# Performance work log

Hardware: AMD Instinct MI355X
Metric: run time of the kernel (lower is better)

Reference implementation:

```python
import jax, jax.numpy as jnp
import numpy as np

N, C, T, V = 128, 256, 64, 32
FILTERS = 256

def setup_inputs() -> dict:
    key = jax.random.key(0)
    k1, k2, k3 = jax.random.split(key, 3)
    x = jax.random.normal(k1, (N, C, T, V), dtype=jnp.float32)
    a = jax.random.uniform(k2, (N, T, V, V), dtype=jnp.float32)
    # 1x1 Conv2D (channels_first) == pointwise channel projection: weight [C_in, filters]
    W = jax.random.normal(k3, (C, FILTERS), dtype=jnp.float32) * (2.0 / FILTERS) ** 0.5
    b = jnp.zeros((FILTERS,), dtype=jnp.float32)
    return {"x": x, "a": a, "W": W, "b": b}

def reference(x, a, W, b):
    # 1x1 conv over channels_first input: [n,c,t,v] -> [n,f,t,v]
    h = jnp.einsum('nctv,cf->nftv', x, W) + b[None, :, None, None]
    # Dropout is identity at inference (training=False).
    # Per-frame graph convolution: contract vertex dim with adjacency.
    out = jnp.einsum('nctv,ntvw->nctw', h, a)
    return (out, a)
```

## Files before the change

kernel.cpp:

```cpp
#include <hip/hip_runtime.h>


#define NN 128
#define CC 256
#define TT 64
#define VV 32
#define FF 256
#define TB 4

typedef _Float16 half8 __attribute__((ext_vector_type(8)));
typedef _Float16 half4 __attribute__((ext_vector_type(4)));
typedef float floatx4 __attribute__((ext_vector_type(4)));

__global__ __launch_bounds__(256) void wt_prep_kernel(const float* __restrict__ W,
                                                      _Float16* __restrict__ Wt) {
    const int c = blockIdx.x;
    const int f = threadIdx.x;
    Wt[f * CC + c] = (_Float16)W[c * FF + f];
}

__global__ __launch_bounds__(512, 2) void sgcn_mfma10_kernel(
    const float* __restrict__ x, const float* __restrict__ a,
    const _Float16* __restrict__ Wt, const float* __restrict__ b,
    float* __restrict__ out, float* __restrict__ out_a)
{
    __shared__ _Float16 a_t[TB * VV * VV];
    __shared__ _Float16 g_s[TB * VV * 256];
    __shared__ float    s_lds[TB][VV];

    const int tid  = threadIdx.x;
    const int lane = tid & 63;
    const int wv   = tid >> 6;
    const int l15  = lane & 15;
    const int lg   = lane >> 4;
    const int blk  = blockIdx.x;
    const int n    = blk >> 4;
    const int t0   = (blk & 15) * TB;

    char* at_base = (char*)a_t;
    char* g_base  = (char*)g_s;

    const int tA    = wv >> 1;
    const int chalf = wv & 1;

    float4 xf[16];
    #pragma unroll
    for (int ci = 0; ci < 8; ++ci) {
        const int c = (chalf * 8 + ci) * 16 + l15;
        const float* xp = x + (((size_t)n * CC + c) * TT + (t0 + tA)) * VV + 8 * lg;
        xf[ci * 2 + 0] = *reinterpret_cast<const float4*>(xp);
        xf[ci * 2 + 1] = *reinterpret_cast<const float4*>(xp + 4);
    }

    #pragma unroll
    for (int k = 0; k < 2; ++k) {
        const int o  = (tid + 512 * k) * 4;
        const int it = o >> 10;
        const int r  = o & 1023;
        const int v  = r >> 5;
        const int w0 = r & 31;
        const size_t off = ((size_t)(n * TT + t0 + it)) * (VV * VV) + r;
        float4 av = *reinterpret_cast<const float4*>(a + off);
        *reinterpret_cast<float4*>(out_a + off) = av;
        #pragma unroll
        for (int j = 0; j < 4; ++j) {
            const int row = it * VV + w0 + j;
            const float e = j == 0 ? av.x : j == 1 ? av.y : j == 2 ? av.z : av.w;
            *reinterpret_cast<_Float16*>(at_base + row * 64 +
                                         ((v * 2) ^ ((row & 3) << 4))) = (_Float16)e;
        }
    }

    __syncthreads();

    if (tid < TB * VV) {
        const int it = tid >> 5, w = tid & 31;
        const int row = it * VV + w;
        float ss = 0.0f;
        #pragma unroll
        for (int v = 0; v < VV; ++v)
            ss += (float)*reinterpret_cast<const _Float16*>(
                at_base + row * 64 + ((v * 2) ^ ((row & 3) << 4)));
        s_lds[it][w] = ss;
    }

    {
        const int r0 = tA * VV + l15, r1 = r0 + 16;
        half8 bA0 = *reinterpret_cast<const half8*>(at_base + r0 * 64 +
                                                    ((16 * lg) ^ ((r0 & 3) << 4)));
        half8 bA1 = *reinterpret_cast<const half8*>(at_base + r1 * 64 +
                                                    ((16 * lg) ^ ((r1 & 3) << 4)));
        char* gt = g_base + tA * (VV * 256 * 2);
        #pragma unroll
        for (int ci = 0; ci < 8; ++ci) {
            const int ct = chalf * 8 + ci;
            half8 af;
            float4 x0 = xf[ci * 2 + 0], x1 = xf[ci * 2 + 1];
            af[0] = (_Float16)x0.x; af[1] = (_Float16)x0.y;
            af[2] = (_Float16)x0.z; af[3] = (_Float16)x0.w;
            af[4] = (_Float16)x1.x; af[5] = (_Float16)x1.y;
            af[6] = (_Float16)x1.z; af[7] = (_Float16)x1.w;
            #pragma unroll
            for (int wt = 0; wt < 2; ++wt) {
                floatx4 acc = {0.f, 0.f, 0.f, 0.f};
                acc = __builtin_amdgcn_mfma_f32_16x16x32_f16(af, wt ? bA1 : bA0, acc, 0, 0, 0);
                half4 gh;
                gh[0] = (_Float16)acc[0]; gh[1] = (_Float16)acc[1];
                gh[2] = (_Float16)acc[2]; gh[3] = (_Float16)acc[3];
                const int row = 16 * wt + l15;
                const int cb  = (ct * 16 + 4 * lg) * 2;
                *reinterpret_cast<half4*>(gt + row * 512 + (cb ^ ((row & 7) << 4))) = gh;
            }
        }
    }
    __syncthreads();

    #pragma unroll
    for (int fth = 0; fth < 2; ++fth) {
        const int ft = fth * 8 + wv;
        const int f  = ft * 16 + l15;
        half8 wb[8];
        const _Float16* wp = Wt + (size_t)f * CC + 8 * lg;
        #pragma unroll
        for (int ks = 0; ks < 8; ++ks)
            wb[ks] = *reinterpret_cast<const half8*>(wp + 32 * ks);
        const float bvf = b[f];

        #pragma unroll
        for (int tt = 0; tt < TB; ++tt) {
            char* gt = g_base + tt * (VV * 256 * 2);
            floatx4 acc2[2];
            acc2[0] = (floatx4){0.f, 0.f, 0.f, 0.f};
            acc2[1] = (floatx4){0.f, 0.f, 0.f, 0.f};

            __builtin_amdgcn_s_setprio(1);
            #pragma unroll
            for (int ks = 0; ks < 8; ++ks) {
                const int r0 = l15, r1 = 16 + l15;
                const int cb = (32 * ks + 8 * lg) * 2;
                half8 ga0 = *reinterpret_cast<const half8*>(gt + r0 * 512 +
                                                            (cb ^ ((r0 & 7) << 4)));
                half8 ga1 = *reinterpret_cast<const half8*>(gt + r1 * 512 +
                                                            (cb ^ ((r1 & 7) << 4)));
                acc2[0] = __builtin_amdgcn_mfma_f32_16x16x32_f16(ga0, wb[ks], acc2[0], 0, 0, 0);
                acc2[1] = __builtin_amdgcn_mfma_f32_16x16x32_f16(ga1, wb[ks], acc2[1], 0, 0, 0);
            }
            __builtin_amdgcn_s_setprio(0);

            float* ob = out + (((size_t)n * FF + f) * TT + (t0 + tt)) * VV;
            #pragma unroll
            for (int mt = 0; mt < 2; ++mt) {
                const int w0 = 16 * mt + 4 * lg;
                float4 sv = *reinterpret_cast<const float4*>(&s_lds[tt][w0]);
                float4 o;
                o.x = acc2[mt][0] + bvf * sv.x;
                o.y = acc2[mt][1] + bvf * sv.y;
                o.z = acc2[mt][2] + bvf * sv.z;
                o.w = acc2[mt][3] + bvf * sv.w;
                *reinterpret_cast<float4*>(ob + w0) = o;
            }
        }
    }
}

__global__ __launch_bounds__(256) void sgcn_fused_kernel(
    const float* __restrict__ x, const float* __restrict__ a,
    const float* __restrict__ W, const float* __restrict__ b,
    float* __restrict__ out, float* __restrict__ out_a)
{
    __shared__ float x_lds[CC][VV];
    __shared__ float a_lds[VV][VV];
    const int tid = threadIdx.x;
    const int nt  = blockIdx.x;
    const int n   = nt >> 6;
    const int t   = nt & 63;
    const float* xb = x + (size_t)n * CC * TT * VV + (size_t)t * VV;
    #pragma unroll
    for (int k = 0; k < 8; ++k) {
        int e = tid * 4 + k * 1024;
        int c = e >> 5, v = e & 31;
        float4 val = *reinterpret_cast<const float4*>(xb + (size_t)c * (TT * VV) + v);
        *reinterpret_cast<float4*>(&x_lds[c][v]) = val;
    }
    {
        const float* ab = a + (size_t)nt * (VV * VV);
        float4 av = *reinterpret_cast<const float4*>(ab + tid * 4);
        *reinterpret_cast<float4*>(&a_lds[0][0] + tid * 4) = av;
        *reinterpret_cast<float4*>(out_a + (size_t)nt * (VV * VV) + tid * 4) = av;
    }
    __syncthreads();
    const int f = tid;
    float h[VV];
    #pragma unroll
    for (int v = 0; v < VV; ++v) h[v] = 0.0f;
    #pragma unroll 4
    for (int c = 0; c < CC; ++c) {
        float wv = W[c * FF + f];
        #pragma unroll
        for (int v = 0; v < VV; ++v) h[v] = fmaf(x_lds[c][v], wv, h[v]);
    }
    const float bias = b[f];
    #pragma unroll
    for (int v = 0; v < VV; ++v) h[v] += bias;
    float o[VV];
    #pragma unroll
    for (int w = 0; w < VV; ++w) o[w] = 0.0f;
    #pragma unroll
    for (int v = 0; v < VV; ++v) {
        float hv = h[v];
        #pragma unroll
        for (int w = 0; w < VV; ++w) o[w] = fmaf(hv, a_lds[v][w], o[w]);
    }
    float* ob = out + (((size_t)n * FF + f) * TT + t) * VV;
    #pragma unroll
    for (int w = 0; w < VV; w += 4)
        *reinterpret_cast<float4*>(ob + w) = make_float4(o[w], o[w+1], o[w+2], o[w+3]);
}

extern "C" void kernel_launch(void* const* d_in, const int* in_sizes, int n_in,
                              void* d_out, int out_size, void* d_ws, size_t ws_size,
                              hipStream_t stream) {
    const float* x = (const float*)d_in[0];
    const float* a = (const float*)d_in[1];
    const float* W = (const float*)d_in[2];
    const float* b = (const float*)d_in[3];

    float* out   = (float*)d_out;
    float* out_a = out + (size_t)NN * FF * TT * VV;

    const size_t wt_bytes = (size_t)FF * CC * sizeof(_Float16);

    if (ws_size >= wt_bytes) {
        _Float16* Wt = (_Float16*)d_ws;
        wt_prep_kernel<<<dim3(CC), dim3(FF), 0, stream>>>(W, Wt);
        sgcn_mfma10_kernel<<<dim3(NN * (TT / TB)), dim3(512), 0, stream>>>(x, a, Wt, b, out, out_a);
    } else {
        sgcn_fused_kernel<<<dim3(NN * TT), dim3(256), 0, stream>>>(x, a, W, b, out, out_a);
    }
}
```

Measured before the change: 145.7 us.

## Make blocks persistent over four time chunks with software-prefetched x and adjacency loads

Each block now loops over four consecutive time-chunks instead of handling one. Half of the next chunk's x tile and its adjacency tile are prefetched into registers while the current chunk's second GEMM runs, so global-load latency overlaps with MFMA work. The grid shrinks fourfold (512 blocks), which lowers launch parallelism and may reduce latency hiding on a large GPU. W fragments are still reloaded for every chunk, and the extra prefetch registers raise register pressure.

```diff
diff --git a/kernel.cpp b/kernel.cpp
--- a/kernel.cpp
+++ b/kernel.cpp
@@ -7,6 +7,7 @@
 #define VV 32
 #define FF 256
 #define TB 4
+#define NCH 4
 
 typedef _Float16 half8 __attribute__((ext_vector_type(8)));
 typedef _Float16 half4 __attribute__((ext_vector_type(4)));
@@ -19,14 +20,14 @@
     Wt[f * CC + c] = (_Float16)W[c * FF + f];
 }
 
-__global__ __launch_bounds__(512, 2) void sgcn_mfma10_kernel(
+__global__ __launch_bounds__(512, 2) void sgcn_mfma12_kernel(
     const float* __restrict__ x, const float* __restrict__ a,
     const _Float16* __restrict__ Wt, const float* __restrict__ b,
     float* __restrict__ out, float* __restrict__ out_a)
 {
     __shared__ _Float16 a_t[TB * VV * VV];
     __shared__ _Float16 g_s[TB * VV * 256];
-    __shared__ float    s_lds[TB][VV];
+    __shared__ float    s_buf[2][TB][VV];
 
     const int tid  = threadIdx.x;
     const int lane = tid & 63;
@@ -34,8 +35,8 @@
     const int l15  = lane & 15;
     const int lg   = lane >> 4;
     const int blk  = blockIdx.x;
-    const int n    = blk >> 4;
-    const int t0   = (blk & 15) * TB;
+    const int n    = blk >> 2;
+    const int tgb  = (blk & 3) * NCH;
 
     char* at_base = (char*)a_t;
     char* g_base  = (char*)g_s;
@@ -43,121 +44,160 @@
     const int tA    = wv >> 1;
     const int chalf = wv & 1;
 
-    float4 xf[16];
-    #pragma unroll
-    for (int ci = 0; ci < 8; ++ci) {
-        const int c = (chalf * 8 + ci) * 16 + l15;
-        const float* xp = x + (((size_t)n * CC + c) * TT + (t0 + tA)) * VV + 8 * lg;
-        xf[ci * 2 + 0] = *reinterpret_cast<const float4*>(xp);
-        xf[ci * 2 + 1] = *reinterpret_cast<const float4*>(xp + 4);
-    }
-
-    #pragma unroll
-    for (int k = 0; k < 2; ++k) {
-        const int o  = (tid + 512 * k) * 4;
-        const int it = o >> 10;
-        const int r  = o & 1023;
-        const int v  = r >> 5;
-        const int w0 = r & 31;
-        const size_t off = ((size_t)(n * TT + t0 + it)) * (VV * VV) + r;
-        float4 av = *reinterpret_cast<const float4*>(a + off);
-        *reinterpret_cast<float4*>(out_a + off) = av;
-        #pragma unroll
-        for (int j = 0; j < 4; ++j) {
-            const int row = it * VV + w0 + j;
-            const float e = j == 0 ? av.x : j == 1 ? av.y : j == 2 ? av.z : av.w;
-            *reinterpret_cast<_Float16*>(at_base + row * 64 +
-                                         ((v * 2) ^ ((row & 3) << 4))) = (_Float16)e;
-        }
-    }
-
-    __syncthreads();
-
-    if (tid < TB * VV) {
-        const int it = tid >> 5, w = tid & 31;
-        const int row = it * VV + w;
-        float ss = 0.0f;
-        #pragma unroll
-        for (int v = 0; v < VV; ++v)
-            ss += (float)*reinterpret_cast<const _Float16*>(
-                at_base + row * 64 + ((v * 2) ^ ((row & 3) << 4)));
-        s_lds[it][w] = ss;
-    }
-
+    const int o0  = tid * 4;
+    const int o1  = (tid + 512) * 4;
+    const int it0 = o0 >> 10, r0s = o0 & 1023;
+    const int it1 = o1 >> 10, r1s = o1 & 1023;
+
+    float4 a_nx[2];
+    float4 xp[8];
     {
-        const int r0 = tA * VV + l15, r1 = r0 + 16;
-        half8 bA0 = *reinterpret_cast<const half8*>(at_base + r0 * 64 +
-                                                    ((16 * lg) ^ ((r0 & 3) << 4)));
-        half8 bA1 = *reinterpret_cast<const half8*>(at_base + r1 * 64 +
-                                                    ((16 * lg) ^ ((r1 & 3) << 4)));
-        char* gt = g_base + tA * (VV * 256 * 2);
-        #pragma unroll
-        for (int ci = 0; ci < 8; ++ci) {
-            const int ct = chalf * 8 + ci;
-            half8 af;
-            float4 x0 = xf[ci * 2 + 0], x1 = xf[ci * 2 + 1];
-            af[0] = (_Float16)x0.x; af[1] = (_Float16)x0.y;
-            af[2] = (_Float16)x0.z; af[3] = (_Float16)x0.w;
-            af[4] = (_Float16)x1.x; af[5] = (_Float16)x1.y;
-            af[6] = (_Float16)x1.z; af[7] = (_Float16)x1.w;
-            #pragma unroll
-            for (int wt = 0; wt < 2; ++wt) {
-                floatx4 acc = {0.f, 0.f, 0.f, 0.f};
-                acc = __builtin_amdgcn_mfma_f32_16x16x32_f16(af, wt ? bA1 : bA0, acc, 0, 0, 0);
-                half4 gh;
-                gh[0] = (_Float16)acc[0]; gh[1] = (_Float16)acc[1];
-                gh[2] = (_Float16)acc[2]; gh[3] = (_Float16)acc[3];
-                const int row = 16 * wt + l15;
-                const int cb  = (ct * 16 + 4 * lg) * 2;
-                *reinterpret_cast<half4*>(gt + row * 512 + (cb ^ ((row & 7) << 4))) = gh;
-            }
-        }
-    }
-    __syncthreads();
-
-    #pragma unroll
-    for (int fth = 0; fth < 2; ++fth) {
-        const int ft = fth * 8 + wv;
-        const int f  = ft * 16 + l15;
-        half8 wb[8];
-        const _Float16* wp = Wt + (size_t)f * CC + 8 * lg;
-        #pragma unroll
-        for (int ks = 0; ks < 8; ++ks)
-            wb[ks] = *reinterpret_cast<const half8*>(wp + 32 * ks);
-        const float bvf = b[f];
-
-        #pragma unroll
-        for (int tt = 0; tt < TB; ++tt) {
-            char* gt = g_base + tt * (VV * 256 * 2);
-            floatx4 acc2[2];
-            acc2[0] = (floatx4){0.f, 0.f, 0.f, 0.f};
-            acc2[1] = (floatx4){0.f, 0.f, 0.f, 0.f};
-
-            __builtin_amdgcn_s_setprio(1);
-            #pragma unroll
-            for (int ks = 0; ks < 8; ++ks) {
-                const int r0 = l15, r1 = 16 + l15;
-                const int cb = (32 * ks + 8 * lg) * 2;
-                half8 ga0 = *reinterpret_cast<const half8*>(gt + r0 * 512 +
-                                                            (cb ^ ((r0 & 7) << 4)));
-                half8 ga1 = *reinterpret_cast<const half8*>(gt + r1 * 512 +
-                                                            (cb ^ ((r1 & 7) << 4)));
-                acc2[0] = __builtin_amdgcn_mfma_f32_16x16x32_f16(ga0, wb[ks], acc2[0], 0, 0, 0);
-                acc2[1] = __builtin_amdgcn_mfma_f32_16x16x32_f16(ga1, wb[ks], acc2[1], 0, 0, 0);
-            }
-            __builtin_amdgcn_s_setprio(0);
-
-            float* ob = out + (((size_t)n * FF + f) * TT + (t0 + tt)) * VV;
-            #pragma unroll
-            for (int mt = 0; mt < 2; ++mt) {
-                const int w0 = 16 * mt + 4 * lg;
-                float4 sv = *reinterpret_cast<const float4*>(&s_lds[tt][w0]);
-                float4 o;
-                o.x = acc2[mt][0] + bvf * sv.x;
-                o.y = acc2[mt][1] + bvf * sv.y;
-                o.z = acc2[mt][2] + bvf * sv.z;
-                o.w = acc2[mt][3] + bvf * sv.w;
-                *reinterpret_cast<float4*>(ob + w0) = o;
+        const int t0 = tgb * TB;
+        a_nx[0] = *reinterpret_cast<const float4*>(a + ((size_t)(n * TT + t0 + it0)) * 1024 + r0s);
+        a_nx[1] = *reinterpret_cast<const float4*>(a + ((size_t)(n * TT + t0 + it1)) * 1024 + r1s);
+        #pragma unroll
+        for (int ci = 0; ci < 4; ++ci) {
+            const int c = (chalf * 8 + ci) * 16 + l15;
+            const float* xpp = x + (((size_t)n * CC + c) * TT + (t0 + tA)) * VV + 8 * lg;
+            xp[ci * 2 + 0] = *reinterpret_cast<const float4*>(xpp);
+            xp[ci * 2 + 1] = *reinterpret_cast<const float4*>(xpp + 4);
+        }
+    }
+
+    #pragma unroll 1
+    for (int ch = 0; ch < NCH; ++ch) {
+        const int t0 = (tgb + ch) * TB;
+
+        float4 xb[8];
+        #pragma unroll
+        for (int ci = 4; ci < 8; ++ci) {
+            const int c = (chalf * 8 + ci) * 16 + l15;
+            const float* xpp = x + (((size_t)n * CC + c) * TT + (t0 + tA)) * VV + 8 * lg;
+            xb[(ci - 4) * 2 + 0] = *reinterpret_cast<const float4*>(xpp);
+            xb[(ci - 4) * 2 + 1] = *reinterpret_cast<const float4*>(xpp + 4);
+        }
+
+        #pragma unroll
+        for (int k = 0; k < 2; ++k) {
+            const int it = k == 0 ? it0 : it1;
+            const int rr = k == 0 ? r0s : r1s;
+            const int v  = rr >> 5;
+            const int w0 = rr & 31;
+            const size_t off = ((size_t)(n * TT + t0 + it)) * 1024 + rr;
+            float4 av = a_nx[k];
+            *reinterpret_cast<float4*>(out_a + off) = av;
+            #pragma unroll
+            for (int j = 0; j < 4; ++j) {
+                const int row = it * VV + w0 + j;
+                const float e = j == 0 ? av.x : j == 1 ? av.y : j == 2 ? av.z : av.w;
+                *reinterpret_cast<_Float16*>(at_base + row * 64 +
+                                             ((v * 2) ^ ((row & 3) << 4))) = (_Float16)e;
+            }
+        }
+
+        __syncthreads();
+
+        if (tid < TB * VV) {
+            const int it = tid >> 5, w = tid & 31;
+            const int row = it * VV + w;
+            float ss = 0.0f;
+            #pragma unroll
+            for (int v = 0; v < VV; ++v)
+                ss += (float)*reinterpret_cast<const _Float16*>(
+                    at_base + row * 64 + ((v * 2) ^ ((row & 3) << 4)));
+            s_buf[ch & 1][it][w] = ss;
+        }
+
+        {
+            const int ra = tA * VV + l15, rb = ra + 16;
+            half8 bA0 = *reinterpret_cast<const half8*>(at_base + ra * 64 +
+                                                        ((16 * lg) ^ ((ra & 3) << 4)));
+            half8 bA1 = *reinterpret_cast<const half8*>(at_base + rb * 64 +
+                                                        ((16 * lg) ^ ((rb & 3) << 4)));
+            char* gt = g_base + tA * (VV * 256 * 2);
+            #pragma unroll
+            for (int ci = 0; ci < 8; ++ci) {
+                const int ct = chalf * 8 + ci;
+                float4 x0 = ci < 4 ? xp[ci * 2 + 0] : xb[(ci - 4) * 2 + 0];
+                float4 x1 = ci < 4 ? xp[ci * 2 + 1] : xb[(ci - 4) * 2 + 1];
+                half8 af;
+                af[0] = (_Float16)x0.x; af[1] = (_Float16)x0.y;
+                af[2] = (_Float16)x0.z; af[3] = (_Float16)x0.w;
+                af[4] = (_Float16)x1.x; af[5] = (_Float16)x1.y;
+                af[6] = (_Float16)x1.z; af[7] = (_Float16)x1.w;
+                #pragma unroll
+                for (int wt = 0; wt < 2; ++wt) {
+                    floatx4 acc = {0.f, 0.f, 0.f, 0.f};
+                    acc = __builtin_amdgcn_mfma_f32_16x16x32_f16(af, wt ? bA1 : bA0, acc, 0, 0, 0);
+                    half4 gh;
+                    gh[0] = (_Float16)acc[0]; gh[1] = (_Float16)acc[1];
+                    gh[2] = (_Float16)acc[2]; gh[3] = (_Float16)acc[3];
+                    const int row = 16 * wt + l15;
+                    const int cb  = (ct * 16 + 4 * lg) * 2;
+                    *reinterpret_cast<half4*>(gt + row * 512 + (cb ^ ((row & 7) << 4))) = gh;
+                }
+            }
+        }
+
+        if (ch + 1 < NCH) {
+            const int t0n = (tgb + ch + 1) * TB;
+            a_nx[0] = *reinterpret_cast<const float4*>(a + ((size_t)(n * TT + t0n + it0)) * 1024 + r0s);
+            a_nx[1] = *reinterpret_cast<const float4*>(a + ((size_t)(n * TT + t0n + it1)) * 1024 + r1s);
+            #pragma unroll
+            for (int ci = 0; ci < 4; ++ci) {
+                const int c = (chalf * 8 + ci) * 16 + l15;
+                const float* xpp = x + (((size_t)n * CC + c) * TT + (t0n + tA)) * VV + 8 * lg;
+                xp[ci * 2 + 0] = *reinterpret_cast<const float4*>(xpp);
+                xp[ci * 2 + 1] = *reinterpret_cast<const float4*>(xpp + 4);
+            }
+        }
+
+        __syncthreads();
+
+        #pragma unroll
+        for (int fth = 0; fth < 2; ++fth) {
+            const int ft = fth * 8 + wv;
+            const int f  = ft * 16 + l15;
+            half8 wb[8];
+            const _Float16* wp = Wt + (size_t)f * CC + 8 * lg;
+            #pragma unroll
+            for (int ks = 0; ks < 8; ++ks)
+                wb[ks] = *reinterpret_cast<const half8*>(wp + 32 * ks);
+            const float bvf = b[f];
+
+            #pragma unroll
+            for (int tt = 0; tt < TB; ++tt) {
+                char* gt = g_base + tt * (VV * 256 * 2);
+                floatx4 acc2[2];
+                acc2[0] = (floatx4){0.f, 0.f, 0.f, 0.f};
+                acc2[1] = (floatx4){0.f, 0.f, 0.f, 0.f};
+
+                __builtin_amdgcn_s_setprio(1);
+                #pragma unroll
+                for (int ks = 0; ks < 8; ++ks) {
+                    const int rr0 = l15, rr1 = 16 + l15;
+                    const int cb = (32 * ks + 8 * lg) * 2;
+                    half8 ga0 = *reinterpret_cast<const half8*>(gt + rr0 * 512 +
+                                                                (cb ^ ((rr0 & 7) << 4)));
+                    half8 ga1 = *reinterpret_cast<const half8*>(gt + rr1 * 512 +
+                                                                (cb ^ ((rr1 & 7) << 4)));
+                    acc2[0] = __builtin_amdgcn_mfma_f32_16x16x32_f16(ga0, wb[ks], acc2[0], 0, 0, 0);
+                    acc2[1] = __builtin_amdgcn_mfma_f32_16x16x32_f16(ga1, wb[ks], acc2[1], 0, 0, 0);
+                }
+                __builtin_amdgcn_s_setprio(0);
+
+                float* ob = out + (((size_t)n * FF + f) * TT + (t0 + tt)) * VV;
+                #pragma unroll
+                for (int mt = 0; mt < 2; ++mt) {
+                    const int w0 = 16 * mt + 4 * lg;
+                    float4 sv = *reinterpret_cast<const float4*>(&s_buf[ch & 1][tt][w0]);
+                    float4 o;
+                    o.x = acc2[mt][0] + bvf * sv.x;
+                    o.y = acc2[mt][1] + bvf * sv.y;
+                    o.z = acc2[mt][2] + bvf * sv.z;
+                    o.w = acc2[mt][3] + bvf * sv.w;
+                    *reinterpret_cast<float4*>(ob + w0) = o;
+                }
             }
         }
     }
@@ -233,7 +273,7 @@
     if (ws_size >= wt_bytes) {
         _Float16* Wt = (_Float16*)d_ws;
         wt_prep_kernel<<<dim3(CC), dim3(FF), 0, stream>>>(W, Wt);
-        sgcn_mfma10_kernel<<<dim3(NN * (TT / TB)), dim3(512), 0, stream>>>(x, a, Wt, b, out, out_a);
+        sgcn_mfma12_kernel<<<dim3(NN * (TT / (TB * NCH))), dim3(512), 0, stream>>>(x, a, Wt, b, out, out_a);
     } else {
         sgcn_fused_kernel<<<dim3(NN * TT), dim3(256), 0, stream>>>(x, a, W, b, out, out_a);
     }
```

After: 152.9 us. 1.05x slower.
